# Kernel optimization log

Hardware: AMD Instinct MI355X
Metric: run time of the kernel (lower is better)

Reference implementation:

```python
import jax, jax.numpy as jnp
import numpy as np

IN_FEATURES = 1024
OUT_FEATURES = 1024
THRESHOLD = 0.05


def ternary_quantize(x, threshold):
    # {-1, 0, +1}: zero where |x| < threshold, else sign(x)
    return jnp.where(jnp.abs(x) < threshold, jnp.zeros_like(x), jnp.sign(x))


def setup_inputs() -> dict:
    key = jax.random.key(0)
    kx, kw = jax.random.split(key)
    x = jax.random.normal(kx, (32768, IN_FEATURES), dtype=jnp.float32)
    # xavier_uniform for weight [out, in]: bound = sqrt(6/(fan_in+fan_out))
    bound = float(np.sqrt(6.0 / (IN_FEATURES + OUT_FEATURES)))
    weight = jax.random.uniform(kw, (OUT_FEATURES, IN_FEATURES), dtype=jnp.float32,
                                minval=-bound, maxval=bound)
    return {"x": x, "weight": weight}


def reference(x, weight):
    x_tern = ternary_quantize(x, THRESHOLD).astype(jnp.int8)
    w_tern = ternary_quantize(weight, THRESHOLD).astype(jnp.int8)
    # int32 accumulate matmul: [T, in] @ [in, out] -> [T, out]
    out = jnp.matmul(x_tern.astype(jnp.int32), w_tern.astype(jnp.int32).T)
    return out.astype(jnp.float32)
```

## Files before the change

### kernel.cpp

```cpp
#include <hip/hip_runtime.h>

#define THRESH 0.05f

typedef __attribute__((ext_vector_type(4))) int   int32x4;
typedef __attribute__((ext_vector_type(4))) float floatx4;

__global__ __launch_bounds__(256) void quant_w_kernel(const float* __restrict__ w,
                                                      signed char* __restrict__ wqf) {
    int c = blockIdx.x * 256 + threadIdx.x;
    int l15  = c & 15;
    int quad = (c >> 4) & 3;
    int nb   = (c >> 6) & 63;
    int kb   = c >> 12;
    int col   = nb * 16 + l15;
    int kbase = kb * 64 + quad * 16;
    const float* src = w + col * 1024 + kbase;
    signed char q[16];
    #pragma unroll
    for (int j = 0; j < 4; ++j) {
        float4 f = *(const float4*)(src + j * 4);
        q[j * 4 + 0] = (signed char)((f.x >= THRESH) - (f.x <= -THRESH));
        q[j * 4 + 1] = (signed char)((f.y >= THRESH) - (f.y <= -THRESH));
        q[j * 4 + 2] = (signed char)((f.z >= THRESH) - (f.z <= -THRESH));
        q[j * 4 + 3] = (signed char)((f.w >= THRESH) - (f.w <= -THRESH));
    }
    *(int32x4*)(wqf + (size_t)c * 16) = *(const int32x4*)q;
}

__global__ __launch_bounds__(256, 4) void tern_gemm_kernel(const float* __restrict__ x,
                                                           const signed char* __restrict__ wqf,
                                                           float* __restrict__ out) {
    __shared__ __attribute__((aligned(16))) signed char a_lds[32 * 1024];
    const int tid = threadIdx.x;
    const long rowbase = (long)blockIdx.x * 32;

    #pragma unroll
    for (int i = 0; i < 8; ++i) {
        int c   = tid + i * 256;
        int row = c >> 6;
        int cir = c & 63;
        const floatx4* src = (const floatx4*)(x + (rowbase + row) * 1024 + cir * 16);
        signed char q[16];
        #pragma unroll
        for (int j = 0; j < 4; ++j) {
            floatx4 f = __builtin_nontemporal_load(src + j);
            #pragma unroll
            for (int e = 0; e < 4; ++e)
                q[j * 4 + e] = (signed char)((f[e] >= THRESH) - (f[e] <= -THRESH));
        }
        int swz = (cir ^ (row & 7)) * 16;
        *(int32x4*)(a_lds + row * 1024 + swz) = *(const int32x4*)q;
    }
    __syncthreads();

    const int wave = tid >> 6;
    const int lane = tid & 63;
    const int l15  = lane & 15;
    const int lq   = lane >> 4;

    for (int colit = 0; colit < 16; ++colit) {
        const int nb = colit * 4 + wave;

        int32x4 bf[16];
        #pragma unroll
        for (int k = 0; k < 16; ++k)
            bf[k] = *(const int32x4*)(wqf + (size_t)(k * 64 + nb) * 1024 + lane * 16);
        __builtin_amdgcn_sched_barrier(0);

        int32x4 acc[2];
        acc[0] = (int32x4){0, 0, 0, 0};
        acc[1] = (int32x4){0, 0, 0, 0};

        #pragma unroll
        for (int k = 0; k < 16; ++k) {
            const int kchunk = k * 4 + lq;
            #pragma unroll
            for (int ri = 0; ri < 2; ++ri) {
                int m = ri * 16 + l15;
                int32x4 af = *(const int32x4*)(a_lds + m * 1024 + ((kchunk ^ (m & 7)) * 16));
                acc[ri] = __builtin_amdgcn_mfma_i32_16x16x64_i8(bf[k], af, acc[ri], 0, 0, 0);
            }
        }

        const int cb = colit * 64 + wave * 16;
        #pragma unroll
        for (int ri = 0; ri < 2; ++ri) {
            const long row = rowbase + ri * 16 + l15;
            floatx4 v;
            v[0] = (float)acc[ri][0];
            v[1] = (float)acc[ri][1];
            v[2] = (float)acc[ri][2];
            v[3] = (float)acc[ri][3];
            __builtin_nontemporal_store(v, (floatx4*)(out + row * 1024 + cb + lq * 4));
        }
    }
}

extern "C" void kernel_launch(void* const* d_in, const int* in_sizes, int n_in,
                              void* d_out, int out_size, void* d_ws, size_t ws_size,
                              hipStream_t stream) {
    const float* x = (const float*)d_in[0];
    const float* w = (const float*)d_in[1];
    float* out = (float*)d_out;
    signed char* wqf = (signed char*)d_ws;

    quant_w_kernel<<<dim3(256), dim3(256), 0, stream>>>(w, wqf);
    tern_gemm_kernel<<<dim3(1024), dim3(256), 0, stream>>>(x, wqf, out);
}
```

Measured before the change: 288.1 us.

## Pre-quantize activations and stream tiles into LDS with global_load_lds

Splits activation quantization into its own kernel that writes swizzled int8 rows to workspace. A new GEMM kernel then loads 64-row A tiles and per-k B slices straight into LDS with global_load_lds, and computes a 64x256 output tile per block with 512 threads. The aim is to raise reuse of the B operand and to remove per-lane global loads of B into registers. In exchange it adds a 32 MB int8 round trip through HBM and two barriers per k-step with no double buffering, and keeps the old kernel as a fallback when workspace is too small.

```diff
diff --git a/kernel.cpp b/kernel.cpp
--- a/kernel.cpp
+++ b/kernel.cpp
@@ -4,6 +4,11 @@
 
 typedef __attribute__((ext_vector_type(4))) int   int32x4;
 typedef __attribute__((ext_vector_type(4))) float floatx4;
+
+typedef __attribute__((address_space(1))) const void global_cvoid;
+typedef __attribute__((address_space(3))) void lds_void;
+
+#define GLLDS16(gp, lp) __builtin_amdgcn_global_load_lds((global_cvoid*)(gp), (lds_void*)(lp), 16, 0, 0)
 
 __global__ __launch_bounds__(256) void quant_w_kernel(const float* __restrict__ w,
                                                       signed char* __restrict__ wqf) {
@@ -12,9 +17,7 @@
     int quad = (c >> 4) & 3;
     int nb   = (c >> 6) & 63;
     int kb   = c >> 12;
-    int col   = nb * 16 + l15;
-    int kbase = kb * 64 + quad * 16;
-    const float* src = w + col * 1024 + kbase;
+    const float* src = w + (nb * 16 + l15) * 1024 + kb * 64 + quad * 16;
     signed char q[16];
     #pragma unroll
     for (int j = 0; j < 4; ++j) {
@@ -27,9 +30,105 @@
     *(int32x4*)(wqf + (size_t)c * 16) = *(const int32x4*)q;
 }
 
-__global__ __launch_bounds__(256, 4) void tern_gemm_kernel(const float* __restrict__ x,
-                                                           const signed char* __restrict__ wqf,
-                                                           float* __restrict__ out) {
+__global__ __launch_bounds__(256) void quant_x_kernel(const float* __restrict__ x,
+                                                      signed char* __restrict__ xq) {
+    size_t c = (size_t)blockIdx.x * 256 + threadIdx.x;
+    int row = (int)(c >> 6);
+    int cir = (int)(c & 63);
+    const floatx4* src = (const floatx4*)(x + c * 16);
+    signed char q[16];
+    #pragma unroll
+    for (int j = 0; j < 4; ++j) {
+        floatx4 f = __builtin_nontemporal_load(src + j);
+        #pragma unroll
+        for (int e = 0; e < 4; ++e)
+            q[j * 4 + e] = (signed char)((f[e] >= THRESH) - (f[e] <= -THRESH));
+    }
+    *(int32x4*)(xq + (size_t)row * 1024 + (cir ^ (row & 7)) * 16) = *(const int32x4*)q;
+}
+
+__global__ __launch_bounds__(512, 4) void tern_gemm_dma(const signed char* __restrict__ xq,
+                                                        const signed char* __restrict__ wqf,
+                                                        float* __restrict__ out) {
+    __shared__ __attribute__((aligned(16))) signed char a_lds[64 * 1024];
+    __shared__ __attribute__((aligned(16))) signed char b_lds[16 * 1024];
+
+    const int tid  = threadIdx.x;
+    const int wave = tid >> 6;
+    const int lane = tid & 63;
+    const int l15  = lane & 15;
+    const int lq   = lane >> 4;
+    const int rh   = wave & 1;
+    const int cq   = wave >> 1;
+
+    const int rowslab = blockIdx.x & 511;
+    const int colq    = blockIdx.x >> 9;
+    const long rowbase = (long)rowslab * 64;
+
+    {
+        const signed char* asrc = xq + rowbase * 1024;
+        #pragma unroll
+        for (int r = 0; r < 8; ++r)
+            GLLDS16(asrc + r * 8192 + tid * 16, a_lds + r * 8192 + wave * 1024);
+        const signed char* bsrc = wqf + (size_t)(colq * 16) * 1024;
+        #pragma unroll
+        for (int r = 0; r < 2; ++r)
+            GLLDS16(bsrc + r * 8192 + tid * 16, b_lds + r * 8192 + wave * 1024);
+    }
+    __syncthreads();
+
+    int32x4 acc[2][4];
+    #pragma unroll
+    for (int ri = 0; ri < 2; ++ri)
+        #pragma unroll
+        for (int ci = 0; ci < 4; ++ci)
+            acc[ri][ci] = (int32x4){0, 0, 0, 0};
+
+    for (int kc = 0; kc < 16; ++kc) {
+        const int kchunk = kc * 4 + lq;
+        int32x4 bf[4];
+        #pragma unroll
+        for (int ci = 0; ci < 4; ++ci)
+            bf[ci] = *(const int32x4*)(b_lds + (cq * 4 + ci) * 1024 + lane * 16);
+        #pragma unroll
+        for (int ri = 0; ri < 2; ++ri) {
+            const int m = rh * 32 + ri * 16 + l15;
+            int32x4 af = *(const int32x4*)(a_lds + m * 1024 + ((kchunk ^ (m & 7)) * 16));
+            #pragma unroll
+            for (int ci = 0; ci < 4; ++ci)
+                acc[ri][ci] = __builtin_amdgcn_mfma_i32_16x16x64_i8(
+                    bf[ci], af, acc[ri][ci], 0, 0, 0);
+        }
+
+        __syncthreads();
+        if (kc < 15) {
+            const signed char* bsrc = wqf + (size_t)((kc + 1) * 64 + colq * 16) * 1024;
+            #pragma unroll
+            for (int r = 0; r < 2; ++r)
+                GLLDS16(bsrc + r * 8192 + tid * 16, b_lds + r * 8192 + wave * 1024);
+        }
+        __syncthreads();
+    }
+
+    #pragma unroll
+    for (int ri = 0; ri < 2; ++ri) {
+        const long row = rowbase + rh * 32 + ri * 16 + l15;
+        #pragma unroll
+        for (int ci = 0; ci < 4; ++ci) {
+            floatx4 v;
+            v[0] = (float)acc[ri][ci][0];
+            v[1] = (float)acc[ri][ci][1];
+            v[2] = (float)acc[ri][ci][2];
+            v[3] = (float)acc[ri][ci][3];
+            const int col = colq * 256 + cq * 64 + ci * 16 + lq * 4;
+            __builtin_nontemporal_store(v, (floatx4*)(out + row * 1024 + col));
+        }
+    }
+}
+
+__global__ __launch_bounds__(256, 4) void tern_gemm_fb(const float* __restrict__ x,
+                                                       const signed char* __restrict__ wqf,
+                                                       float* __restrict__ out) {
     __shared__ __attribute__((aligned(16))) signed char a_lds[32 * 1024];
     const int tid = threadIdx.x;
     const long rowbase = (long)blockIdx.x * 32;
@@ -48,8 +147,7 @@
             for (int e = 0; e < 4; ++e)
                 q[j * 4 + e] = (signed char)((f[e] >= THRESH) - (f[e] <= -THRESH));
         }
-        int swz = (cir ^ (row & 7)) * 16;
-        *(int32x4*)(a_lds + row * 1024 + swz) = *(const int32x4*)q;
+        *(int32x4*)(a_lds + row * 1024 + (cir ^ (row & 7)) * 16) = *(const int32x4*)q;
     }
     __syncthreads();
 
@@ -60,12 +158,10 @@
 
     for (int colit = 0; colit < 16; ++colit) {
         const int nb = colit * 4 + wave;
-
         int32x4 bf[16];
         #pragma unroll
         for (int k = 0; k < 16; ++k)
             bf[k] = *(const int32x4*)(wqf + (size_t)(k * 64 + nb) * 1024 + lane * 16);
-        __builtin_amdgcn_sched_barrier(0);
 
         int32x4 acc[2];
         acc[0] = (int32x4){0, 0, 0, 0};
@@ -105,5 +201,13 @@
     signed char* wqf = (signed char*)d_ws;
 
     quant_w_kernel<<<dim3(256), dim3(256), 0, stream>>>(w, wqf);
-    tern_gemm_kernel<<<dim3(1024), dim3(256), 0, stream>>>(x, wqf, out);
-}
+
+    const size_t need = (1u << 20) + (size_t)32768 * 1024;
+    if (ws_size >= need) {
+        signed char* xq = (signed char*)d_ws + (1u << 20);
+        quant_x_kernel<<<dim3(8192), dim3(256), 0, stream>>>(x, xq);
+        tern_gemm_dma<<<dim3(2048), dim3(512), 0, stream>>>(xq, wqf, out);
+    } else {
+        tern_gemm_fb<<<dim3(1024), dim3(256), 0, stream>>>(x, wqf, out);
+    }
+}
```

Result: slower. 298.4 us (+3.6%).
